# Performance work log

Hardware: AMD Instinct MI355X
Metric: run time of the kernel (lower is better)

The kernel has to match this reference:

```python
import jax, jax.numpy as jnp
import numpy as np

GRID = 8          # proto_grid
EPS = 1e-4        # safe_norm eps
TAU = 20.0        # temperature used throughout


def avg_pool(x, k):
    # non-overlapping avg pool, kernel k divides H and W exactly
    S, C, H, W = x.shape
    return x.reshape(S, C, H // k, k, W // k, k).mean(axis=(3, 5))


def safe_norm(x, axis):
    n = jnp.sqrt(jnp.sum(x * x, axis=axis, keepdims=True))
    return x / jnp.maximum(n, EPS)


def setup_inputs() -> dict:
    key = jax.random.key(0)
    k1, k2, k3 = jax.random.split(key, 3)
    qry = jax.random.normal(k1, (1, 1, 256, 128, 128), dtype=jnp.float32)
    sup_x = jax.random.normal(k2, (1, 5, 1, 256, 128, 128), dtype=jnp.float32)
    sup_y = jax.random.uniform(k3, (1, 5, 1, 128, 128), dtype=jnp.float32)
    return {"qry": qry, "sup_x": sup_x, "sup_y": sup_y, "thresh": 0}


def reference(qry, sup_x, sup_y, thresh):
    # mode == 'gridconv', use_cross_attn=False, isval=False
    qry = qry[:, 0]          # squeeze(1)        -> [1, 256, 128, 128]
    sup_x = sup_x[0, :, 0]   # squeeze(0,2)      -> [5, 256, 128, 128]
    sup_y = sup_y[0]         # squeeze(0)        -> [5, 1, 128, 128]

    shot, nc, H, W = sup_x.shape
    k = H // GRID

    # grid prototypes: avgpool then [shot, nc, g*g] -> [shot, g*g, nc] -> [shot*g*g, nc]
    n_sup = avg_pool(sup_x, k)
    protos = n_sup.reshape(shot, nc, -1).transpose(0, 2, 1).reshape(-1, nc)
    # selection mask: avg_pool(sup_y) > thresh. sup_y is uniform(0,1) and
    # thresh=0, so every grid cell is selected -> selection is the identity
    # (fixed-shape, jit-safe; matches the torch boolean index exactly here).

    # mean-center then safe L2-normalize (channel dim)
    protos = protos - protos.mean(axis=-1, keepdims=True)
    qryc = qry - qry.mean(axis=1, keepdims=True)
    pro_n = safe_norm(protos, axis=1)        # [npro, nc]
    qry_n = safe_norm(qryc, axis=1)          # [b, nc, h, w]

    # 1x1 conv as cosine similarity against prototype bank
    dists = jnp.einsum('bchw,pc->bphw', qry_n, pro_n) * TAU   # [b, npro, h, w]
    prob = jax.nn.softmax(dists, axis=1)
    # bmm combine: channel-wise weighted prototypes per pixel
    ch_proto = jnp.einsum('pc,bphw->bchw', pro_n, prob)       # [b, nc, h, w]
    pred_grid = jnp.sum(qry_n * ch_proto * TAU, axis=1, keepdims=True)

    debug_assign = jnp.argmax(dists, axis=1).astype(jnp.float32)
    return pred_grid, debug_assign
```

## Files before the change

### kernel.cpp

```cpp
#include <hip/hip_runtime.h>

#define NCH   256
#define NPROT 320
#define HW    16384
#define TAU   20.0f
#define EPSN  1e-4f

typedef _Float16 half8 __attribute__((ext_vector_type(8)));
typedef float    f32x4 __attribute__((ext_vector_type(4)));

__global__ __launch_bounds__(256) void k_pool(const float* __restrict__ sup_x,
                                              float* __restrict__ praw) {
    int b = blockIdx.x;
    int t = threadIdx.x;
    const float4* plane = (const float4*)(sup_x + (size_t)b * HW);
    float rsum[8];
    #pragma unroll
    for (int r = 0; r < 8; ++r) rsum[r] = 0.f;
    #pragma unroll
    for (int i = 0; i < 16; ++i) {
        float4 v = plane[i * 256 + t];
        rsum[i >> 1] += v.x + v.y + v.z + v.w;
    }
    __shared__ float part[8][256];
    #pragma unroll
    for (int r = 0; r < 8; ++r) part[r][t] = rsum[r];
    __syncthreads();
    int R  = t >> 5;
    int cw = t & 31;
    float s = 0.f;
    #pragma unroll
    for (int a = 0; a < 8; ++a) s += part[R][a * 32 + cw];
    s += __shfl_xor(s, 1);
    s += __shfl_xor(s, 2);
    if ((t & 3) == 0) {
        int shot = b >> 8, c = b & 255;
        int p = shot * 64 + R * 8 + (cw >> 2);
        praw[(size_t)p * NCH + c] = s * (1.0f / 256.0f);
    }
}

__device__ __forceinline__ float block_sum256(float x, float* ws4, int t) {
    #pragma unroll
    for (int o = 1; o < 64; o <<= 1) x += __shfl_xor(x, o);
    if ((t & 63) == 0) ws4[t >> 6] = x;
    __syncthreads();
    float r = ws4[0] + ws4[1] + ws4[2] + ws4[3];
    __syncthreads();
    return r;
}

__global__ __launch_bounds__(256) void k_norm(const float* __restrict__ praw,
                                              _Float16* __restrict__ PTh,
                                              _Float16* __restrict__ PTl,
                                              float* __restrict__ sp) {
    int p = blockIdx.x;
    int c = threadIdx.x;
    __shared__ float ws4[4];
    float v = praw[p * NCH + c];
    float mean = block_sum256(v, ws4, c) * (1.0f / 256.0f);
    float cen = v - mean;
    float n2 = block_sum256(cen * cen, ws4, c);
    float inv = 1.0f / fmaxf(sqrtf(n2), EPSN);
    float pn = cen * inv;
    _Float16 hi = (_Float16)pn;
    float lo = (pn - (float)hi) * 2048.0f;
    size_t idx = ((size_t)(c >> 3) * NPROT + p) * 8 + (c & 7);
    PTh[idx] = hi;
    PTl[idx] = (_Float16)lo;
    float ssum = block_sum256(pn, ws4, c);
    if (c == 0) sp[p] = ssum;
}

__global__ __launch_bounds__(256, 2) void k_main(const float* __restrict__ qry,
                                                 const _Float16* __restrict__ PTh,
                                                 const _Float16* __restrict__ PTl,
                                                 const float* __restrict__ sp,
                                                 float* __restrict__ out) {
    __shared__ __align__(16) _Float16 Ah[32 * 256];
    __shared__ __align__(16) _Float16 Al[32 * 256];
    __shared__ float red1[32 * 33], red2[32 * 33];
    __shared__ float meanv[32], invnv[32];
    __shared__ float Mw[4][32], Sw[4][32], Tw[4][32], Iw[4][32];
    int t = threadIdx.x;
    int pixbase = blockIdx.x * 32;

    {
        int f4 = t & 7;
        int c0 = t >> 3;
        float ps1[4] = {0.f, 0.f, 0.f, 0.f};
        float ps2[4] = {0.f, 0.f, 0.f, 0.f};
        char* AhB = (char*)Ah;
        char* AlB = (char*)Al;
        #pragma unroll
        for (int i = 0; i < 8; ++i) {
            int c = c0 + 32 * i;
            float4 v = *(const float4*)(qry + (size_t)c * HW + pixbase + f4 * 4);
            float q[4] = {v.x, v.y, v.z, v.w};
            #pragma unroll
            for (int j = 0; j < 4; ++j) {
                int px = f4 * 4 + j;
                float x = q[j];
                _Float16 h = (_Float16)x;
                _Float16 l = (_Float16)((x - (float)h) * 2048.0f);
                int off = px * 512 + ((2 * c) ^ ((px & 7) << 4));
                *(_Float16*)(AhB + off) = h;
                *(_Float16*)(AlB + off) = l;
                ps1[j] += x;
                ps2[j] = fmaf(x, x, ps2[j]);
            }
        }
        #pragma unroll
        for (int j = 0; j < 4; ++j) {
            red1[c0 * 33 + f4 * 4 + j] = ps1[j];
            red2[c0 * 33 + f4 * 4 + j] = ps2[j];
        }
    }
    __syncthreads();
    if (t < 32) {
        float s1 = 0.f, s2 = 0.f;
        #pragma unroll
        for (int j = 0; j < 32; ++j) { s1 += red1[j * 33 + t]; s2 += red2[j * 33 + t]; }
        float mean = s1 * (1.0f / 256.0f);
        float n2 = fmaxf(s2 - s1 * mean, 0.f);
        meanv[t] = mean;
        invnv[t] = 1.0f / fmaxf(sqrtf(n2), EPSN);
    }
    __syncthreads();

    int lane = t & 63, w = t >> 6;
    int col = lane & 15, g4 = lane >> 4;
    int aswz = (col & 7) << 4;
    const char* AhB = (const char*)Ah + col * 512;
    const char* AlB = (const char*)Al + col * 512;
    const half8* BH = (const half8*)PTh;
    const half8* BL = (const half8*)PTl;

    f32x4 dva[2][5];
    float spv[5];

    #pragma unroll
    for (int nt = 0; nt < 5; ++nt) {
        int nb = w * 80 + nt * 16 + col;
        spv[nt] = sp[nb];
        f32x4 a1_0 = {0.f, 0.f, 0.f, 0.f}, a1_1 = {0.f, 0.f, 0.f, 0.f};
        f32x4 a2_0 = {0.f, 0.f, 0.f, 0.f}, a2_1 = {0.f, 0.f, 0.f, 0.f};
        half8 bh0 = BH[(0 * 4 + g4) * 320 + nb];
        half8 bl0 = BL[(0 * 4 + g4) * 320 + nb];
        half8 bh1 = BH[(1 * 4 + g4) * 320 + nb];
        half8 bl1 = BL[(1 * 4 + g4) * 320 + nb];
        #pragma unroll 2
        for (int kb = 0; kb < 8; ++kb) {
            half8 bhn{}, bln{};
            if (kb < 6) {
                bhn = BH[((kb + 2) * 4 + g4) * 320 + nb];
                bln = BL[((kb + 2) * 4 + g4) * 320 + nb];
            }
            int koff = (kb * 64 + g4 * 16) ^ aswz;
            half8 ah0 = *(const half8*)(AhB + koff);
            half8 ah1 = *(const half8*)(AhB + koff + 8192);
            half8 al0 = *(const half8*)(AlB + koff);
            half8 al1 = *(const half8*)(AlB + koff + 8192);
            a1_0 = __builtin_amdgcn_mfma_f32_16x16x32_f16(ah0, bh0, a1_0, 0, 0, 0);
            a1_1 = __builtin_amdgcn_mfma_f32_16x16x32_f16(ah1, bh0, a1_1, 0, 0, 0);
            a2_0 = __builtin_amdgcn_mfma_f32_16x16x32_f16(ah0, bl0, a2_0, 0, 0, 0);
            a2_0 = __builtin_amdgcn_mfma_f32_16x16x32_f16(al0, bh0, a2_0, 0, 0, 0);
            a2_1 = __builtin_amdgcn_mfma_f32_16x16x32_f16(ah1, bl0, a2_1, 0, 0, 0);
            a2_1 = __builtin_amdgcn_mfma_f32_16x16x32_f16(al1, bh0, a2_1, 0, 0, 0);
            bh0 = bh1; bl0 = bl1;
            bh1 = bhn; bl1 = bln;
        }
        dva[0][nt] = a1_0 + a2_0 * (1.0f / 2048.0f);
        dva[1][nt] = a1_1 + a2_1 * (1.0f / 2048.0f);
    }

    #pragma unroll
    for (int mt = 0; mt < 2; ++mt) {
        #pragma unroll
        for (int r = 0; r < 4; ++r) {
            int pixel = mt * 16 + g4 * 4 + r;
            float mean = meanv[pixel], invn = invnv[pixel];
            float dv[5];
            #pragma unroll
            for (int nt = 0; nt < 5; ++nt)
                dv[nt] = TAU * invn * (dva[mt][nt][r] - mean * spv[nt]);
            float gm = dv[0];
            float gi = (float)(w * 80 + col);
            #pragma unroll
            for (int nt = 1; nt < 5; ++nt)
                if (dv[nt] > gm) { gm = dv[nt]; gi = (float)(w * 80 + nt * 16 + col); }
            #pragma unroll
            for (int o = 1; o < 16; o <<= 1) {
                float om = __shfl_xor(gm, o);
                float oi = __shfl_xor(gi, o);
                if (om > gm || (om == gm && oi < gi)) { gm = om; gi = oi; }
            }
            float S = 0.f, T = 0.f;
            #pragma unroll
            for (int nt = 0; nt < 5; ++nt) {
                float e = __expf(dv[nt] - gm);
                S += e;
                T = fmaf(e, dv[nt], T);
            }
            #pragma unroll
            for (int o = 1; o < 16; o <<= 1) { S += __shfl_xor(S, o); T += __shfl_xor(T, o); }
            if (col == 0) { Mw[w][pixel] = gm; Sw[w][pixel] = S; Tw[w][pixel] = T; Iw[w][pixel] = gi; }
        }
    }
    __syncthreads();

    if (t < 32) {
        float gm = Mw[0][t], gi = Iw[0][t];
        #pragma unroll
        for (int k = 1; k < 4; ++k)
            if (Mw[k][t] > gm) { gm = Mw[k][t]; gi = Iw[k][t]; }
        float S = 0.f, T = 0.f;
        #pragma unroll
        for (int k = 0; k < 4; ++k) {
            float sc = __expf(Mw[k][t] - gm);
            S = fmaf(Sw[k][t], sc, S);
            T = fmaf(Tw[k][t], sc, T);
        }
        out[pixbase + t] = T / S;
        out[HW + pixbase + t] = gi;
    }
}

extern "C" void kernel_launch(void* const* d_in, const int* in_sizes, int n_in,
                              void* d_out, int out_size, void* d_ws, size_t ws_size,
                              hipStream_t stream) {
    const float* qry   = (const float*)d_in[0];
    const float* sup_x = (const float*)d_in[1];
    float* out = (float*)d_out;

    float* praw   = (float*)d_ws;
    _Float16* PTh = (_Float16*)(praw + NPROT * NCH);
    _Float16* PTl = PTh + NPROT * NCH;
    float* sp     = (float*)(PTl + NPROT * NCH);

    k_pool<<<5 * 256, 256, 0, stream>>>(sup_x, praw);
    k_norm<<<NPROT, 256, 0, stream>>>(praw, PTh, PTl, sp);
    k_main<<<HW / 32, 256, 0, stream>>>(qry, PTh, PTl, sp, out);
}
```

Before: 160.3 us.

## Shrink main tile to 16 pixels, prenormalize query, swizzle block order

Each k_main block now covers 16 pixels instead of 32, which doubles the grid and raises the occupancy hint to 4 blocks per CU. The query values are kept in registers, mean-centred and normalised before the fp16 hi/lo split, so the per-prototype sum correction (sp) is no longer needed in the epilogue. Blocks are remapped with a strided tile order, and the manual B-operand prefetch is dropped in favour of a fully unrolled loop. Each B fragment is now used for only one M tile instead of two, so prototype-bank traffic per pixel doubles.

Result: no change. 159.4 us (-0.5%).

```diff
diff --git a/kernel.cpp b/kernel.cpp
--- a/kernel.cpp
+++ b/kernel.cpp
@@ -72,59 +72,70 @@
     if (c == 0) sp[p] = ssum;
 }
 
-__global__ __launch_bounds__(256, 2) void k_main(const float* __restrict__ qry,
+__global__ __launch_bounds__(256, 4) void k_main(const float* __restrict__ qry,
                                                  const _Float16* __restrict__ PTh,
                                                  const _Float16* __restrict__ PTl,
-                                                 const float* __restrict__ sp,
                                                  float* __restrict__ out) {
-    __shared__ __align__(16) _Float16 Ah[32 * 256];
-    __shared__ __align__(16) _Float16 Al[32 * 256];
-    __shared__ float red1[32 * 33], red2[32 * 33];
-    __shared__ float meanv[32], invnv[32];
-    __shared__ float Mw[4][32], Sw[4][32], Tw[4][32], Iw[4][32];
+    __shared__ __align__(16) _Float16 Ah[16 * 256];
+    __shared__ __align__(16) _Float16 Al[16 * 256];
+    __shared__ __align__(16) float red1[64 * 16];
+    __shared__ __align__(16) float red2[64 * 16];
+    __shared__ float meanv[16], invnv[16];
+    __shared__ float Mw[4][16], Sw[4][16], Tw[4][16], Iw[4][16];
     int t = threadIdx.x;
-    int pixbase = blockIdx.x * 32;
-
+    int bid = blockIdx.x;
+    int tile = (bid & 7) * 128 + (bid >> 3);
+    int pixbase = tile * 16;
+
+    int f4 = t & 3;
+    int c0 = t >> 2;
+    float qv[4][4];
     {
-        int f4 = t & 7;
-        int c0 = t >> 3;
         float ps1[4] = {0.f, 0.f, 0.f, 0.f};
         float ps2[4] = {0.f, 0.f, 0.f, 0.f};
-        char* AhB = (char*)Ah;
-        char* AlB = (char*)Al;
-        #pragma unroll
-        for (int i = 0; i < 8; ++i) {
-            int c = c0 + 32 * i;
+        #pragma unroll
+        for (int i = 0; i < 4; ++i) {
+            int c = c0 + 64 * i;
             float4 v = *(const float4*)(qry + (size_t)c * HW + pixbase + f4 * 4);
-            float q[4] = {v.x, v.y, v.z, v.w};
-            #pragma unroll
-            for (int j = 0; j < 4; ++j) {
-                int px = f4 * 4 + j;
-                float x = q[j];
-                _Float16 h = (_Float16)x;
-                _Float16 l = (_Float16)((x - (float)h) * 2048.0f);
-                int off = px * 512 + ((2 * c) ^ ((px & 7) << 4));
-                *(_Float16*)(AhB + off) = h;
-                *(_Float16*)(AlB + off) = l;
-                ps1[j] += x;
-                ps2[j] = fmaf(x, x, ps2[j]);
-            }
-        }
-        #pragma unroll
-        for (int j = 0; j < 4; ++j) {
-            red1[c0 * 33 + f4 * 4 + j] = ps1[j];
-            red2[c0 * 33 + f4 * 4 + j] = ps2[j];
-        }
-    }
-    __syncthreads();
-    if (t < 32) {
+            qv[i][0] = v.x; qv[i][1] = v.y; qv[i][2] = v.z; qv[i][3] = v.w;
+            ps1[0] += v.x; ps2[0] = fmaf(v.x, v.x, ps2[0]);
+            ps1[1] += v.y; ps2[1] = fmaf(v.y, v.y, ps2[1]);
+            ps1[2] += v.z; ps2[2] = fmaf(v.z, v.z, ps2[2]);
+            ps1[3] += v.w; ps2[3] = fmaf(v.w, v.w, ps2[3]);
+        }
+        *(float4*)&red1[c0 * 16 + f4 * 4] = *(float4*)ps1;
+        *(float4*)&red2[c0 * 16 + f4 * 4] = *(float4*)ps2;
+    }
+    __syncthreads();
+    if (t < 16) {
         float s1 = 0.f, s2 = 0.f;
         #pragma unroll
-        for (int j = 0; j < 32; ++j) { s1 += red1[j * 33 + t]; s2 += red2[j * 33 + t]; }
+        for (int j = 0; j < 64; ++j) { s1 += red1[j * 16 + t]; s2 += red2[j * 16 + t]; }
         float mean = s1 * (1.0f / 256.0f);
         float n2 = fmaxf(s2 - s1 * mean, 0.f);
         meanv[t] = mean;
         invnv[t] = 1.0f / fmaxf(sqrtf(n2), EPSN);
+    }
+    __syncthreads();
+
+    {
+        char* AhB = (char*)Ah;
+        char* AlB = (char*)Al;
+        #pragma unroll
+        for (int j = 0; j < 4; ++j) {
+            int px = f4 * 4 + j;
+            float mean = meanv[px], invn = invnv[px];
+            #pragma unroll
+            for (int i = 0; i < 4; ++i) {
+                int c = c0 + 64 * i;
+                float qn = (qv[i][j] - mean) * invn;
+                _Float16 h = (_Float16)qn;
+                _Float16 l = (_Float16)((qn - (float)h) * 2048.0f);
+                int off = px * 512 + ((2 * c) ^ ((px & 7) << 4));
+                *(_Float16*)(AhB + off) = h;
+                *(_Float16*)(AlB + off) = l;
+            }
+        }
     }
     __syncthreads();
 
@@ -136,80 +147,58 @@
     const half8* BH = (const half8*)PTh;
     const half8* BL = (const half8*)PTl;
 
-    f32x4 dva[2][5];
-    float spv[5];
+    f32x4 dva[5];
 
     #pragma unroll
     for (int nt = 0; nt < 5; ++nt) {
         int nb = w * 80 + nt * 16 + col;
-        spv[nt] = sp[nb];
-        f32x4 a1_0 = {0.f, 0.f, 0.f, 0.f}, a1_1 = {0.f, 0.f, 0.f, 0.f};
-        f32x4 a2_0 = {0.f, 0.f, 0.f, 0.f}, a2_1 = {0.f, 0.f, 0.f, 0.f};
-        half8 bh0 = BH[(0 * 4 + g4) * 320 + nb];
-        half8 bl0 = BL[(0 * 4 + g4) * 320 + nb];
-        half8 bh1 = BH[(1 * 4 + g4) * 320 + nb];
-        half8 bl1 = BL[(1 * 4 + g4) * 320 + nb];
-        #pragma unroll 2
+        f32x4 a1 = {0.f, 0.f, 0.f, 0.f};
+        f32x4 a2 = {0.f, 0.f, 0.f, 0.f};
+        #pragma unroll
         for (int kb = 0; kb < 8; ++kb) {
-            half8 bhn{}, bln{};
-            if (kb < 6) {
-                bhn = BH[((kb + 2) * 4 + g4) * 320 + nb];
-                bln = BL[((kb + 2) * 4 + g4) * 320 + nb];
-            }
+            half8 bh = BH[(kb * 4 + g4) * 320 + nb];
+            half8 bl = BL[(kb * 4 + g4) * 320 + nb];
             int koff = (kb * 64 + g4 * 16) ^ aswz;
-            half8 ah0 = *(const half8*)(AhB + koff);
-            half8 ah1 = *(const half8*)(AhB + koff + 8192);
-            half8 al0 = *(const half8*)(AlB + koff);
-            half8 al1 = *(const half8*)(AlB + koff + 8192);
-            a1_0 = __builtin_amdgcn_mfma_f32_16x16x32_f16(ah0, bh0, a1_0, 0, 0, 0);
-            a1_1 = __builtin_amdgcn_mfma_f32_16x16x32_f16(ah1, bh0, a1_1, 0, 0, 0);
-            a2_0 = __builtin_amdgcn_mfma_f32_16x16x32_f16(ah0, bl0, a2_0, 0, 0, 0);
-            a2_0 = __builtin_amdgcn_mfma_f32_16x16x32_f16(al0, bh0, a2_0, 0, 0, 0);
-            a2_1 = __builtin_amdgcn_mfma_f32_16x16x32_f16(ah1, bl0, a2_1, 0, 0, 0);
-            a2_1 = __builtin_amdgcn_mfma_f32_16x16x32_f16(al1, bh0, a2_1, 0, 0, 0);
-            bh0 = bh1; bl0 = bl1;
-            bh1 = bhn; bl1 = bln;
-        }
-        dva[0][nt] = a1_0 + a2_0 * (1.0f / 2048.0f);
-        dva[1][nt] = a1_1 + a2_1 * (1.0f / 2048.0f);
-    }
-
-    #pragma unroll
-    for (int mt = 0; mt < 2; ++mt) {
-        #pragma unroll
-        for (int r = 0; r < 4; ++r) {
-            int pixel = mt * 16 + g4 * 4 + r;
-            float mean = meanv[pixel], invn = invnv[pixel];
-            float dv[5];
-            #pragma unroll
-            for (int nt = 0; nt < 5; ++nt)
-                dv[nt] = TAU * invn * (dva[mt][nt][r] - mean * spv[nt]);
-            float gm = dv[0];
-            float gi = (float)(w * 80 + col);
-            #pragma unroll
-            for (int nt = 1; nt < 5; ++nt)
-                if (dv[nt] > gm) { gm = dv[nt]; gi = (float)(w * 80 + nt * 16 + col); }
-            #pragma unroll
-            for (int o = 1; o < 16; o <<= 1) {
-                float om = __shfl_xor(gm, o);
-                float oi = __shfl_xor(gi, o);
-                if (om > gm || (om == gm && oi < gi)) { gm = om; gi = oi; }
-            }
-            float S = 0.f, T = 0.f;
-            #pragma unroll
-            for (int nt = 0; nt < 5; ++nt) {
-                float e = __expf(dv[nt] - gm);
-                S += e;
-                T = fmaf(e, dv[nt], T);
-            }
-            #pragma unroll
-            for (int o = 1; o < 16; o <<= 1) { S += __shfl_xor(S, o); T += __shfl_xor(T, o); }
-            if (col == 0) { Mw[w][pixel] = gm; Sw[w][pixel] = S; Tw[w][pixel] = T; Iw[w][pixel] = gi; }
-        }
-    }
-    __syncthreads();
-
-    if (t < 32) {
+            half8 ah = *(const half8*)(AhB + koff);
+            half8 al = *(const half8*)(AlB + koff);
+            a1 = __builtin_amdgcn_mfma_f32_16x16x32_f16(ah, bh, a1, 0, 0, 0);
+            a2 = __builtin_amdgcn_mfma_f32_16x16x32_f16(ah, bl, a2, 0, 0, 0);
+            a2 = __builtin_amdgcn_mfma_f32_16x16x32_f16(al, bh, a2, 0, 0, 0);
+        }
+        dva[nt] = a1 + a2 * (1.0f / 2048.0f);
+    }
+
+    #pragma unroll
+    for (int r = 0; r < 4; ++r) {
+        int pixel = g4 * 4 + r;
+        float dv[5];
+        #pragma unroll
+        for (int nt = 0; nt < 5; ++nt) dv[nt] = TAU * dva[nt][r];
+        float gm = dv[0];
+        float gi = (float)(w * 80 + col);
+        #pragma unroll
+        for (int nt = 1; nt < 5; ++nt)
+            if (dv[nt] > gm) { gm = dv[nt]; gi = (float)(w * 80 + nt * 16 + col); }
+        #pragma unroll
+        for (int o = 1; o < 16; o <<= 1) {
+            float om = __shfl_xor(gm, o);
+            float oi = __shfl_xor(gi, o);
+            if (om > gm || (om == gm && oi < gi)) { gm = om; gi = oi; }
+        }
+        float S = 0.f, T = 0.f;
+        #pragma unroll
+        for (int nt = 0; nt < 5; ++nt) {
+            float e = __expf(dv[nt] - gm);
+            S += e;
+            T = fmaf(e, dv[nt], T);
+        }
+        #pragma unroll
+        for (int o = 1; o < 16; o <<= 1) { S += __shfl_xor(S, o); T += __shfl_xor(T, o); }
+        if (col == 0) { Mw[w][pixel] = gm; Sw[w][pixel] = S; Tw[w][pixel] = T; Iw[w][pixel] = gi; }
+    }
+    __syncthreads();
+
+    if (t < 16) {
         float gm = Mw[0][t], gi = Iw[0][t];
         #pragma unroll
         for (int k = 1; k < 4; ++k)
@@ -240,5 +229,5 @@
 
     k_pool<<<5 * 256, 256, 0, stream>>>(sup_x, praw);
     k_norm<<<NPROT, 256, 0, stream>>>(praw, PTh, PTl, sp);
-    k_main<<<HW / 32, 256, 0, stream>>>(qry, PTh, PTl, sp, out);
-}
+    k_main<<<HW / 16, 256, 0, stream>>>(qry, PTh, PTl, out);
+}
```
